# Performance work log

Measured on AMD Instinct MI355X. Metric: run time of the kernel, lower is better.

## Reference

```python
import jax, jax.numpy as jnp
import numpy as np

N_NODES = 50000
N_GRAPHS = 64
VOCAB = 100000
D = 256
PAD_IDX = 0


def setup_inputs() -> dict:
    key = jax.random.key(0)
    ks = jax.random.split(key, 8)
    seq = jax.random.randint(ks[0], (N_NODES, 16), 0, VOCAB)
    edge_index = jax.random.randint(ks[1], (2, 800000), 0, N_NODES)
    batch = jnp.sort(jax.random.randint(ks[2], (N_NODES,), 0, N_GRAPHS))
    emb = jax.random.normal(ks[3], (VOCAB, D), dtype=jnp.float32) * 0.02
    emb = emb.at[PAD_IDX].set(0.0)  # padding_idx row is zero
    W0 = jax.random.normal(ks[4], (D, D), dtype=jnp.float32) * (1.0 / np.sqrt(D))
    b0 = jnp.zeros((D,), dtype=jnp.float32)
    W1 = jax.random.normal(ks[5], (D, D), dtype=jnp.float32) * (1.0 / np.sqrt(D))
    b1 = jnp.zeros((D,), dtype=jnp.float32)
    return {"seq": seq, "edge_index": edge_index, "batch": batch,
            "emb": emb, "W0": W0, "b0": b0, "W1": W1, "b1": b1}


def _gcn_layer(x, W, b, src, dst, dis):
    # GCN with self-loops and symmetric normalization.
    h = x @ W + b  # [N, D]
    norm = dis[src] * dis[dst]  # [E]
    agg = jax.ops.segment_sum(h[src] * norm[:, None], dst, num_segments=N_NODES)
    agg = agg + h * (dis * dis)[:, None]  # self-loop contribution
    return agg


def reference(seq, edge_index, batch, emb, W0, b0, W1, b1):
    # statement encoder: embedding lookup + sum over token parts
    x = jnp.sum(emb[seq], axis=1)  # [N, D]
    src, dst = edge_index[0], edge_index[1]
    # degree with self-loops (counted on destination)
    deg = jax.ops.segment_sum(jnp.ones_like(dst, dtype=x.dtype), dst,
                              num_segments=N_NODES) + 1.0
    dis = jax.lax.rsqrt(deg)  # deg^{-1/2}
    h = _gcn_layer(x, W0, b0, src, dst, dis)
    h = jax.nn.relu(h)
    h = _gcn_layer(h, W1, b1, src, dst, dis)
    out = jax.nn.relu(h)
    # global sum pool over graph ids
    pooled = jax.ops.segment_sum(out, batch, num_segments=N_GRAPHS)  # [G, D]
    return pooled
```

## Files before the change

### kernel.cpp

```cpp
#include <hip/hip_runtime.h>
#include <stdint.h>

#define N_NODES 50000
#define N_GRAPHS 64
#define VOCAB 100000
#define DIM 256
#define N_EDGES 800000
#define T_SEQ 16
#define CAP 64

typedef short bf16x8 __attribute__((ext_vector_type(8)));
typedef unsigned short u16x8 __attribute__((ext_vector_type(8)));
typedef unsigned short u16x4 __attribute__((ext_vector_type(4)));
typedef float f32x4 __attribute__((ext_vector_type(4)));
typedef unsigned short u16;

__device__ __forceinline__ float bf2f(u16 u) {
    union { unsigned int i; float f; } v; v.i = ((unsigned int)u) << 16; return v.f;
}
__device__ __forceinline__ u16 f2bf(float f) {
    union { float f; unsigned int i; } v; v.f = f;
    unsigned int x = v.i;
    return (u16)((x + 0x7fffu + ((x >> 16) & 1u)) >> 16);
}

__device__ __forceinline__ void gload_lds16(const void* g, void* l) {
    __builtin_amdgcn_global_load_lds(
        (const __attribute__((address_space(1))) uint32_t*)g,
        (__attribute__((address_space(3))) uint32_t*)l, 16, 0, 0);
}

__global__ __launch_bounds__(256) void prep_kernel(const float* __restrict__ emb,
        u16* __restrict__ emb_bf, const float* __restrict__ W0, u16* __restrict__ WT0,
        const float* __restrict__ W1, u16* __restrict__ WT1,
        int* __restrict__ counts, float* __restrict__ out) {
    int bid = blockIdx.x;
    if (bid < 12500) {
        size_t base = ((size_t)bid * 256 + threadIdx.x) * 8;
        float4 a = *(const float4*)(emb + base);
        float4 b = *(const float4*)(emb + base + 4);
        ushort4 o0, o1;
        o0.x = f2bf(a.x); o0.y = f2bf(a.y); o0.z = f2bf(a.z); o0.w = f2bf(a.w);
        o1.x = f2bf(b.x); o1.y = f2bf(b.y); o1.z = f2bf(b.z); o1.w = f2bf(b.w);
        *(ushort4*)(emb_bf + base) = o0;
        *(ushort4*)(emb_bf + base + 4) = o1;
        if (bid < 196) {
            int i = bid * 256 + threadIdx.x;
            if (i < N_NODES) counts[i] = 0;
        }
        if (bid < 64) out[bid * 256 + threadIdx.x] = 0.f;
    } else {
        __shared__ u16 tile[32][33];
        int b = bid - 12500;
        int which = b >> 6;
        const float* W = which ? W1 : W0;
        u16* WT = which ? WT1 : WT0;
        b &= 63;
        int bx = b & 7, by = b >> 3;
        int tx = threadIdx.x & 31, ty = threadIdx.x >> 5;
#pragma unroll
        for (int r = 0; r < 32; r += 8)
            tile[ty + r][tx] = f2bf(W[(size_t)(by * 32 + ty + r) * DIM + bx * 32 + tx]);
        __syncthreads();
#pragma unroll
        for (int r = 0; r < 32; r += 8)
            WT[(size_t)(bx * 32 + ty + r) * DIM + by * 32 + tx] = tile[tx][ty + r];
    }
}

__global__ void fill_kernel(const int* __restrict__ src, const int* __restrict__ dst,
        int* __restrict__ counts, u16* __restrict__ bucket) {
    int e = blockIdx.x * 256 + threadIdx.x;
    if (e < N_EDGES) {
        int d = dst[e];
        int p = atomicAdd(&counts[d], 1);
        if (p < CAP) bucket[(size_t)d * CAP + p] = (u16)src[e];
    }
}

__global__ __launch_bounds__(256) void encode_kernel(const int* __restrict__ seq,
        const u16* __restrict__ emb, u16* __restrict__ x) {
    int wave = threadIdx.x >> 6, lane = threadIdx.x & 63;
    int n = blockIdx.x * 4 + wave;
    if (n >= N_NODES) return;
    int half = lane >> 5, l32 = lane & 31;
    int c = l32 * 8;
    int toks[8];
#pragma unroll
    for (int tt = 0; tt < 8; ++tt)
        toks[tt] = seq[n * T_SEQ + half + 2 * tt];
    u16x8 v[8];
#pragma unroll
    for (int tt = 0; tt < 8; ++tt)
        v[tt] = *(const u16x8*)(emb + (size_t)toks[tt] * DIM + c);
    __builtin_amdgcn_sched_barrier(0);
    float a[8] = {0.f, 0.f, 0.f, 0.f, 0.f, 0.f, 0.f, 0.f};
#pragma unroll
    for (int tt = 0; tt < 8; ++tt)
#pragma unroll
        for (int j = 0; j < 8; ++j) a[j] += bf2f(v[tt][j]);
#pragma unroll
    for (int j = 0; j < 8; ++j) a[j] += __shfl_xor(a[j], 32, 64);
    if (half == 0) {
        u16x8 o;
#pragma unroll
        for (int j = 0; j < 8; ++j) o[j] = f2bf(a[j]);
        *(u16x8*)(x + (size_t)n * DIM + c) = o;
    }
}

__global__ __launch_bounds__(256) void gemm_kernel(const u16* __restrict__ A,
        const u16* __restrict__ WT, const float* __restrict__ bias,
        const int* __restrict__ counts, u16* __restrict__ C, int M) {
    __shared__ __align__(16) uint8_t ldsA[128 * 64];
    __shared__ __align__(16) uint8_t ldsB[128 * 64];
    int tid = threadIdx.x;
    int wave = tid >> 6, lane = tid & 63;
    int quad = lane >> 4, l16 = lane & 15;
    int wm = wave & 1, wn = wave >> 1;
    int bm = blockIdx.y * 128, bn = blockIdx.x * 128;

    int srow = wave * 32 + (lane >> 2);
    int sbyte = (lane & 3) * 16;
    uint8_t* dstA = ldsA + wave * 2048;
    uint8_t* dstB = ldsB + wave * 2048;

    f32x4 acc[4][4] = {};

    for (int kt = 0; kt < 8; ++kt) {
        int k0b = kt * 64;
#pragma unroll
        for (int q = 0; q < 2; ++q) {
            int gr = bm + srow + q * 16; if (gr > M - 1) gr = M - 1;
            gload_lds16((const uint8_t*)A + (size_t)gr * (DIM * 2) + k0b + sbyte,
                        dstA + q * 1024);
            int gbr = bn + srow + q * 16;
            gload_lds16((const uint8_t*)WT + (size_t)gbr * (DIM * 2) + k0b + sbyte,
                        dstB + q * 1024);
        }
        __syncthreads();
        bf16x8 afr[4], bfr[4];
#pragma unroll
        for (int t = 0; t < 4; ++t) {
            afr[t] = *(const bf16x8*)(ldsA + (wm * 64 + t * 16 + l16) * 64 + quad * 16);
            bfr[t] = *(const bf16x8*)(ldsB + (wn * 64 + t * 16 + l16) * 64 + quad * 16);
        }
#pragma unroll
        for (int tm = 0; tm < 4; ++tm)
#pragma unroll
            for (int tn = 0; tn < 4; ++tn)
                acc[tm][tn] = __builtin_amdgcn_mfma_f32_16x16x32_bf16(
                    afr[tm], bfr[tn], acc[tm][tn], 0, 0, 0);
        __syncthreads();
    }

    float bv[4];
#pragma unroll
    for (int tn = 0; tn < 4; ++tn) bv[tn] = bias[bn + wn * 64 + tn * 16 + l16];
#pragma unroll
    for (int tm = 0; tm < 4; ++tm) {
        int row0 = bm + wm * 64 + tm * 16 + quad * 4;
#pragma unroll
        for (int r = 0; r < 4; ++r) {
            int row = row0 + r;
            if (row < M) {
                int cnt = counts[row]; if (cnt > CAP) cnt = CAP;
                float dsc = rsqrtf((float)cnt + 1.0f);
#pragma unroll
                for (int tn = 0; tn < 4; ++tn) {
                    int col = bn + wn * 64 + tn * 16 + l16;
                    C[(size_t)row * DIM + col] = f2bf((acc[tm][tn][r] + bv[tn]) * dsc);
                }
            }
        }
    }
}

__global__ __launch_bounds__(256) void agg_kernel(const u16* __restrict__ h,
        const int* __restrict__ counts, const u16* __restrict__ bucket,
        u16* __restrict__ z) {
    int wave = threadIdx.x >> 6, lane = threadIdx.x & 63;
    int n = blockIdx.x * 4 + wave;
    if (n >= N_NODES) return;
    int half = lane >> 5, l32 = lane & 31;
    int c = l32 * 8;
    float a[8];
    if (half == 0) {
        u16x8 v = *(const u16x8*)(h + (size_t)n * DIM + c);
#pragma unroll
        for (int j = 0; j < 8; ++j) a[j] = bf2f(v[j]);
    } else {
#pragma unroll
        for (int j = 0; j < 8; ++j) a[j] = 0.f;
    }
    int cnt = counts[n]; if (cnt > CAP) cnt = CAP;
    const u16* bk = bucket + (size_t)n * CAP;
    int e = half;
    for (; e + 14 < cnt; e += 16) {
        int s0 = bk[e];      int s1 = bk[e + 2];
        int s2 = bk[e + 4];  int s3 = bk[e + 6];
        int s4 = bk[e + 8];  int s5 = bk[e + 10];
        int s6 = bk[e + 12]; int s7 = bk[e + 14];
        u16x8 v0 = *(const u16x8*)(h + (size_t)s0 * DIM + c);
        u16x8 v1 = *(const u16x8*)(h + (size_t)s1 * DIM + c);
        u16x8 v2 = *(const u16x8*)(h + (size_t)s2 * DIM + c);
        u16x8 v3 = *(const u16x8*)(h + (size_t)s3 * DIM + c);
        u16x8 v4 = *(const u16x8*)(h + (size_t)s4 * DIM + c);
        u16x8 v5 = *(const u16x8*)(h + (size_t)s5 * DIM + c);
        u16x8 v6 = *(const u16x8*)(h + (size_t)s6 * DIM + c);
        u16x8 v7 = *(const u16x8*)(h + (size_t)s7 * DIM + c);
        __builtin_amdgcn_sched_barrier(0);
#pragma unroll
        for (int j = 0; j < 8; ++j)
            a[j] += ((bf2f(v0[j]) + bf2f(v1[j])) + (bf2f(v2[j]) + bf2f(v3[j]))) +
                    ((bf2f(v4[j]) + bf2f(v5[j])) + (bf2f(v6[j]) + bf2f(v7[j])));
    }
    for (; e + 6 < cnt; e += 8) {
        int s0 = bk[e];
        int s1 = bk[e + 2];
        int s2 = bk[e + 4];
        int s3 = bk[e + 6];
        u16x8 v0 = *(const u16x8*)(h + (size_t)s0 * DIM + c);
        u16x8 v1 = *(const u16x8*)(h + (size_t)s1 * DIM + c);
        u16x8 v2 = *(const u16x8*)(h + (size_t)s2 * DIM + c);
        u16x8 v3 = *(const u16x8*)(h + (size_t)s3 * DIM + c);
#pragma unroll
        for (int j = 0; j < 8; ++j)
            a[j] += bf2f(v0[j]) + bf2f(v1[j]) + bf2f(v2[j]) + bf2f(v3[j]);
    }
    for (; e < cnt; e += 2) {
        int s = bk[e];
        u16x8 v = *(const u16x8*)(h + (size_t)s * DIM + c);
#pragma unroll
        for (int j = 0; j < 8; ++j) a[j] += bf2f(v[j]);
    }
#pragma unroll
    for (int j = 0; j < 8; ++j) a[j] += __shfl_xor(a[j], 32, 64);
    if (half == 0) {
        float dn = rsqrtf((float)cnt + 1.0f);
        u16x8 o;
#pragma unroll
        for (int j = 0; j < 8; ++j) o[j] = f2bf(fmaxf(a[j] * dn, 0.f));
        *(u16x8*)(z + (size_t)n * DIM + c) = o;
    }
}

__global__ __launch_bounds__(256) void pool_kernel(const u16* __restrict__ z,
        const int* __restrict__ batch, float* __restrict__ out) {
    const int NWAVES = 4096;
    const int NPW = (N_NODES + NWAVES - 1) / NWAVES;
    int gw = blockIdx.x * 4 + (threadIdx.x >> 6);
    int lane = threadIdx.x & 63;
    int n0 = gw * NPW;
    if (n0 >= N_NODES) return;
    int n1 = n0 + NPW; if (n1 > N_NODES) n1 = N_NODES;
    int c = lane * 4;
    float a0 = 0.f, a1 = 0.f, a2 = 0.f, a3 = 0.f;
    int gprev = -1;
    for (int n = n0; n < n1; ++n) {
        int g = batch[n];
        if (g != gprev) {
            if (gprev >= 0) {
                float* o = out + (size_t)gprev * DIM + c;
                atomicAdd(o + 0, a0); atomicAdd(o + 1, a1);
                atomicAdd(o + 2, a2); atomicAdd(o + 3, a3);
            }
            a0 = a1 = a2 = a3 = 0.f; gprev = g;
        }
        u16x4 v = *(const u16x4*)(z + (size_t)n * DIM + c);
        a0 += bf2f(v[0]); a1 += bf2f(v[1]); a2 += bf2f(v[2]); a3 += bf2f(v[3]);
    }
    if (gprev >= 0) {
        float* o = out + (size_t)gprev * DIM + c;
        atomicAdd(o + 0, a0); atomicAdd(o + 1, a1);
        atomicAdd(o + 2, a2); atomicAdd(o + 3, a3);
    }
}

extern "C" void kernel_launch(void* const* d_in, const int* in_sizes, int n_in,
                              void* d_out, int out_size, void* d_ws, size_t ws_size,
                              hipStream_t stream) {
    const int*   seq   = (const int*)d_in[0];
    const int*   eidx  = (const int*)d_in[1];
    const int*   batch = (const int*)d_in[2];
    const float* emb   = (const float*)d_in[3];
    const float* W0    = (const float*)d_in[4];
    const float* b0    = (const float*)d_in[5];
    const float* W1    = (const float*)d_in[6];
    const float* b1    = (const float*)d_in[7];
    float* out = (float*)d_out;

    uint8_t* ws = (uint8_t*)d_ws;
    size_t off = 0;
    auto alloc = [&](size_t bytes) -> uint8_t* {
        uint8_t* p = ws + off;
        off += (bytes + 255) & ~(size_t)255;
        return p;
    };
    u16* emb_bf  = (u16*)alloc((size_t)VOCAB * DIM * 2);
    u16* buf0    = (u16*)alloc((size_t)N_NODES * DIM * 2);
    u16* buf1    = (u16*)alloc((size_t)N_NODES * DIM * 2);
    u16* bucket  = (u16*)alloc((size_t)N_NODES * CAP * 2);
    int* counts  = (int*)alloc((size_t)N_NODES * 4);
    u16* WT0     = (u16*)alloc((size_t)DIM * DIM * 2);
    u16* WT1     = (u16*)alloc((size_t)DIM * DIM * 2);

    const int* esrc = eidx;
    const int* edst = eidx + N_EDGES;

    prep_kernel<<<12500 + 128, 256, 0, stream>>>(emb, emb_bf, W0, WT0, W1, WT1,
                                                 counts, out);
    fill_kernel<<<(N_EDGES + 255) / 256, 256, 0, stream>>>(esrc, edst, counts, bucket);
    encode_kernel<<<(N_NODES + 3) / 4, 256, 0, stream>>>(seq, emb_bf, buf0);

    dim3 ggrid(2, (N_NODES + 127) / 128);
    gemm_kernel<<<ggrid, 256, 0, stream>>>(buf0, WT0, b0, counts, buf1, N_NODES);
    agg_kernel<<<(N_NODES + 3) / 4, 256, 0, stream>>>(buf1, counts, bucket, buf0);
    gemm_kernel<<<ggrid, 256, 0, stream>>>(buf0, WT1, b1, counts, buf1, N_NODES);
    agg_kernel<<<(N_NODES + 3) / 4, 256, 0, stream>>>(buf1, counts, bucket, buf0);

    pool_kernel<<<1024, 256, 0, stream>>>(buf0, batch, out);
}
```

Before: 442.0 us.

## Fuse edge bucketing into prep kernel and fuse final aggregation with pooling

Edge bucket filling now runs as extra blocks inside the prep/cast kernel, and the counts and output zeroing moves to memset calls. The second aggregation is fused with global sum pooling, so each wave aggregates a run of nodes and accumulates per graph in registers instead of writing z and re-reading it. This saves one launch pair and a full N×D round trip. The cost is fewer waves in the fused agg/pool (2048 blocks, several nodes per wave serially), which may reduce latency hiding for the gathers.

```diff
diff --git a/kernel.cpp b/kernel.cpp
--- a/kernel.cpp
+++ b/kernel.cpp
@@ -9,6 +9,13 @@
 #define T_SEQ 16
 #define CAP 64
 
+#define FILL_BLOCKS 3125
+#define CAST_BLOCKS 12500
+#define TRAN_BLOCKS 128
+
+#define AP_BLOCKS 2048
+#define AP_NPW ((N_NODES + AP_BLOCKS * 4 - 1) / (AP_BLOCKS * 4))
+
 typedef short bf16x8 __attribute__((ext_vector_type(8)));
 typedef unsigned short u16x8 __attribute__((ext_vector_type(8)));
 typedef unsigned short u16x4 __attribute__((ext_vector_type(4)));
@@ -30,13 +37,19 @@
         (__attribute__((address_space(3))) uint32_t*)l, 16, 0, 0);
 }
 
-__global__ __launch_bounds__(256) void prep_kernel(const float* __restrict__ emb,
+__global__ __launch_bounds__(256) void prep_fill_kernel(const float* __restrict__ emb,
         u16* __restrict__ emb_bf, const float* __restrict__ W0, u16* __restrict__ WT0,
         const float* __restrict__ W1, u16* __restrict__ WT1,
-        int* __restrict__ counts, float* __restrict__ out) {
+        const int* __restrict__ esrc, const int* __restrict__ edst,
+        int* __restrict__ counts, u16* __restrict__ bucket) {
     int bid = blockIdx.x;
-    if (bid < 12500) {
-        size_t base = ((size_t)bid * 256 + threadIdx.x) * 8;
+    if (bid < FILL_BLOCKS) {
+        int e = bid * 256 + threadIdx.x;
+        int d = edst[e];
+        int p = atomicAdd(&counts[d], 1);
+        if (p < CAP) bucket[(size_t)d * CAP + p] = (u16)esrc[e];
+    } else if (bid < FILL_BLOCKS + CAST_BLOCKS) {
+        size_t base = ((size_t)(bid - FILL_BLOCKS) * 256 + threadIdx.x) * 8;
         float4 a = *(const float4*)(emb + base);
         float4 b = *(const float4*)(emb + base + 4);
         ushort4 o0, o1;
@@ -44,14 +57,9 @@
         o1.x = f2bf(b.x); o1.y = f2bf(b.y); o1.z = f2bf(b.z); o1.w = f2bf(b.w);
         *(ushort4*)(emb_bf + base) = o0;
         *(ushort4*)(emb_bf + base + 4) = o1;
-        if (bid < 196) {
-            int i = bid * 256 + threadIdx.x;
-            if (i < N_NODES) counts[i] = 0;
-        }
-        if (bid < 64) out[bid * 256 + threadIdx.x] = 0.f;
     } else {
         __shared__ u16 tile[32][33];
-        int b = bid - 12500;
+        int b = bid - (FILL_BLOCKS + CAST_BLOCKS);
         int which = b >> 6;
         const float* W = which ? W1 : W0;
         u16* WT = which ? WT1 : WT0;
@@ -65,16 +73,6 @@
 #pragma unroll
         for (int r = 0; r < 32; r += 8)
             WT[(size_t)(bx * 32 + ty + r) * DIM + by * 32 + tx] = tile[tx][ty + r];
-    }
-}
-
-__global__ void fill_kernel(const int* __restrict__ src, const int* __restrict__ dst,
-        int* __restrict__ counts, u16* __restrict__ bucket) {
-    int e = blockIdx.x * 256 + threadIdx.x;
-    if (e < N_EDGES) {
-        int d = dst[e];
-        int p = atomicAdd(&counts[d], 1);
-        if (p < CAP) bucket[(size_t)d * CAP + p] = (u16)src[e];
     }
 }
 
@@ -176,15 +174,9 @@
     }
 }
 
-__global__ __launch_bounds__(256) void agg_kernel(const u16* __restrict__ h,
-        const int* __restrict__ counts, const u16* __restrict__ bucket,
-        u16* __restrict__ z) {
-    int wave = threadIdx.x >> 6, lane = threadIdx.x & 63;
-    int n = blockIdx.x * 4 + wave;
-    if (n >= N_NODES) return;
-    int half = lane >> 5, l32 = lane & 31;
-    int c = l32 * 8;
-    float a[8];
+__device__ __forceinline__ void agg_node(int n, int half, int c,
+        const u16* __restrict__ h, const int* __restrict__ counts,
+        const u16* __restrict__ bucket, float a[8]) {
     if (half == 0) {
         u16x8 v = *(const u16x8*)(h + (size_t)n * DIM + c);
 #pragma unroll
@@ -216,10 +208,8 @@
                     ((bf2f(v4[j]) + bf2f(v5[j])) + (bf2f(v6[j]) + bf2f(v7[j])));
     }
     for (; e + 6 < cnt; e += 8) {
-        int s0 = bk[e];
-        int s1 = bk[e + 2];
-        int s2 = bk[e + 4];
-        int s3 = bk[e + 6];
+        int s0 = bk[e];     int s1 = bk[e + 2];
+        int s2 = bk[e + 4]; int s3 = bk[e + 6];
         u16x8 v0 = *(const u16x8*)(h + (size_t)s0 * DIM + c);
         u16x8 v1 = *(const u16x8*)(h + (size_t)s1 * DIM + c);
         u16x8 v2 = *(const u16x8*)(h + (size_t)s2 * DIM + c);
@@ -236,44 +226,62 @@
     }
 #pragma unroll
     for (int j = 0; j < 8; ++j) a[j] += __shfl_xor(a[j], 32, 64);
+    float dn = rsqrtf((float)cnt + 1.0f);
+#pragma unroll
+    for (int j = 0; j < 8; ++j) a[j] = fmaxf(a[j] * dn, 0.f);
+}
+
+__global__ __launch_bounds__(256) void agg_kernel(const u16* __restrict__ h,
+        const int* __restrict__ counts, const u16* __restrict__ bucket,
+        u16* __restrict__ z) {
+    int wave = threadIdx.x >> 6, lane = threadIdx.x & 63;
+    int n = blockIdx.x * 4 + wave;
+    if (n >= N_NODES) return;
+    int half = lane >> 5, l32 = lane & 31;
+    int c = l32 * 8;
+    float a[8];
+    agg_node(n, half, c, h, counts, bucket, a);
     if (half == 0) {
-        float dn = rsqrtf((float)cnt + 1.0f);
         u16x8 o;
 #pragma unroll
-        for (int j = 0; j < 8; ++j) o[j] = f2bf(fmaxf(a[j] * dn, 0.f));
+        for (int j = 0; j < 8; ++j) o[j] = f2bf(a[j]);
         *(u16x8*)(z + (size_t)n * DIM + c) = o;
     }
 }
 
-__global__ __launch_bounds__(256) void pool_kernel(const u16* __restrict__ z,
+__global__ __launch_bounds__(256) void agg_pool_kernel(const u16* __restrict__ h,
+        const int* __restrict__ counts, const u16* __restrict__ bucket,
         const int* __restrict__ batch, float* __restrict__ out) {
-    const int NWAVES = 4096;
-    const int NPW = (N_NODES + NWAVES - 1) / NWAVES;
     int gw = blockIdx.x * 4 + (threadIdx.x >> 6);
     int lane = threadIdx.x & 63;
-    int n0 = gw * NPW;
+    int half = lane >> 5, l32 = lane & 31;
+    int c = l32 * 8;
+    int n0 = gw * AP_NPW;
     if (n0 >= N_NODES) return;
-    int n1 = n0 + NPW; if (n1 > N_NODES) n1 = N_NODES;
-    int c = lane * 4;
-    float a0 = 0.f, a1 = 0.f, a2 = 0.f, a3 = 0.f;
+    int n1 = n0 + AP_NPW; if (n1 > N_NODES) n1 = N_NODES;
+    float pacc[8] = {0.f, 0.f, 0.f, 0.f, 0.f, 0.f, 0.f, 0.f};
     int gprev = -1;
     for (int n = n0; n < n1; ++n) {
+        float a[8];
+        agg_node(n, half, c, h, counts, bucket, a);
         int g = batch[n];
         if (g != gprev) {
-            if (gprev >= 0) {
+            if (gprev >= 0 && half == 0) {
                 float* o = out + (size_t)gprev * DIM + c;
-                atomicAdd(o + 0, a0); atomicAdd(o + 1, a1);
-                atomicAdd(o + 2, a2); atomicAdd(o + 3, a3);
+#pragma unroll
+                for (int j = 0; j < 8; ++j) atomicAdd(o + j, pacc[j]);
             }
-            a0 = a1 = a2 = a3 = 0.f; gprev = g;
+#pragma unroll
+            for (int j = 0; j < 8; ++j) pacc[j] = 0.f;
+            gprev = g;
         }
-        u16x4 v = *(const u16x4*)(z + (size_t)n * DIM + c);
-        a0 += bf2f(v[0]); a1 += bf2f(v[1]); a2 += bf2f(v[2]); a3 += bf2f(v[3]);
-    }
-    if (gprev >= 0) {
+#pragma unroll
+        for (int j = 0; j < 8; ++j) pacc[j] += a[j];
+    }
+    if (gprev >= 0 && half == 0) {
         float* o = out + (size_t)gprev * DIM + c;
-        atomicAdd(o + 0, a0); atomicAdd(o + 1, a1);
-        atomicAdd(o + 2, a2); atomicAdd(o + 3, a3);
+#pragma unroll
+        for (int j = 0; j < 8; ++j) atomicAdd(o + j, pacc[j]);
     }
 }
 
@@ -308,16 +316,16 @@
     const int* esrc = eidx;
     const int* edst = eidx + N_EDGES;
 
-    prep_kernel<<<12500 + 128, 256, 0, stream>>>(emb, emb_bf, W0, WT0, W1, WT1,
-                                                 counts, out);
-    fill_kernel<<<(N_EDGES + 255) / 256, 256, 0, stream>>>(esrc, edst, counts, bucket);
+    hipMemsetAsync(counts, 0, (size_t)N_NODES * 4, stream);
+    hipMemsetAsync(out, 0, (size_t)N_GRAPHS * DIM * 4, stream);
+
+    prep_fill_kernel<<<FILL_BLOCKS + CAST_BLOCKS + TRAN_BLOCKS, 256, 0, stream>>>(
+        emb, emb_bf, W0, WT0, W1, WT1, esrc, edst, counts, bucket);
     encode_kernel<<<(N_NODES + 3) / 4, 256, 0, stream>>>(seq, emb_bf, buf0);
 
     dim3 ggrid(2, (N_NODES + 127) / 128);
     gemm_kernel<<<ggrid, 256, 0, stream>>>(buf0, WT0, b0, counts, buf1, N_NODES);
     agg_kernel<<<(N_NODES + 3) / 4, 256, 0, stream>>>(buf1, counts, bucket, buf0);
     gemm_kernel<<<ggrid, 256, 0, stream>>>(buf0, WT1, b1, counts, buf1, N_NODES);
-    agg_kernel<<<(N_NODES + 3) / 4, 256, 0, stream>>>(buf1, counts, bucket, buf0);
-
-    pool_kernel<<<1024, 256, 0, stream>>>(buf0, batch, out);
-}
+    agg_pool_kernel<<<AP_BLOCKS, 256, 0, stream>>>(buf1, counts, bucket, batch, out);
+}
```

After: 485.5 us. 9.8% more time.

## Fuse edge bucketing into prep kernel and double-buffer GEMM LDS tiles

Applied to the files above, without the earlier changes.

Merges the edge-bucket fill kernel into the embedding-cast/weight-transpose prep kernel so both run as independent block ranges of one launch. Zeroing of counts and the output moves to hipMemsetAsync calls. The GEMM now double-buffers its LDS A/B tiles, issuing the next k-tile's global-to-LDS loads before computing on the current one, with source addresses hoisted out of the loop. This trades two extra memset launches and twice the LDS per block for fewer kernel launches and overlap of loads with MFMA work. The shown loop no longer has a barrier between issuing the next loads and the MFMAs, so correctness depends on the hidden tail of the loop adding a wait and sync.

```diff
diff --git a/kernel.cpp b/kernel.cpp
--- a/kernel.cpp
+++ b/kernel.cpp
@@ -9,6 +9,10 @@
 #define T_SEQ 16
 #define CAP 64
 
+#define FILL_BLOCKS 3125
+#define CAST_BLOCKS 12500
+#define TRAN_BLOCKS 128
+
 typedef short bf16x8 __attribute__((ext_vector_type(8)));
 typedef unsigned short u16x8 __attribute__((ext_vector_type(8)));
 typedef unsigned short u16x4 __attribute__((ext_vector_type(4)));
@@ -30,13 +34,19 @@
         (__attribute__((address_space(3))) uint32_t*)l, 16, 0, 0);
 }
 
-__global__ __launch_bounds__(256) void prep_kernel(const float* __restrict__ emb,
+__global__ __launch_bounds__(256) void prep_fill_kernel(const float* __restrict__ emb,
         u16* __restrict__ emb_bf, const float* __restrict__ W0, u16* __restrict__ WT0,
         const float* __restrict__ W1, u16* __restrict__ WT1,
-        int* __restrict__ counts, float* __restrict__ out) {
+        const int* __restrict__ esrc, const int* __restrict__ edst,
+        int* __restrict__ counts, u16* __restrict__ bucket) {
     int bid = blockIdx.x;
-    if (bid < 12500) {
-        size_t base = ((size_t)bid * 256 + threadIdx.x) * 8;
+    if (bid < FILL_BLOCKS) {
+        int e = bid * 256 + threadIdx.x;
+        int d = edst[e];
+        int p = atomicAdd(&counts[d], 1);
+        if (p < CAP) bucket[(size_t)d * CAP + p] = (u16)esrc[e];
+    } else if (bid < FILL_BLOCKS + CAST_BLOCKS) {
+        size_t base = ((size_t)(bid - FILL_BLOCKS) * 256 + threadIdx.x) * 8;
         float4 a = *(const float4*)(emb + base);
         float4 b = *(const float4*)(emb + base + 4);
         ushort4 o0, o1;
@@ -44,14 +54,9 @@
         o1.x = f2bf(b.x); o1.y = f2bf(b.y); o1.z = f2bf(b.z); o1.w = f2bf(b.w);
         *(ushort4*)(emb_bf + base) = o0;
         *(ushort4*)(emb_bf + base + 4) = o1;
-        if (bid < 196) {
-            int i = bid * 256 + threadIdx.x;
-            if (i < N_NODES) counts[i] = 0;
-        }
-        if (bid < 64) out[bid * 256 + threadIdx.x] = 0.f;
     } else {
         __shared__ u16 tile[32][33];
-        int b = bid - 12500;
+        int b = bid - (FILL_BLOCKS + CAST_BLOCKS);
         int which = b >> 6;
         const float* W = which ? W1 : W0;
         u16* WT = which ? WT1 : WT0;
@@ -65,16 +70,6 @@
 #pragma unroll
         for (int r = 0; r < 32; r += 8)
             WT[(size_t)(bx * 32 + ty + r) * DIM + by * 32 + tx] = tile[tx][ty + r];
-    }
-}
-
-__global__ void fill_kernel(const int* __restrict__ src, const int* __restrict__ dst,
-        int* __restrict__ counts, u16* __restrict__ bucket) {
-    int e = blockIdx.x * 256 + threadIdx.x;
-    if (e < N_EDGES) {
-        int d = dst[e];
-        int p = atomicAdd(&counts[d], 1);
-        if (p < CAP) bucket[(size_t)d * CAP + p] = (u16)src[e];
     }
 }
 
@@ -112,8 +107,8 @@
 __global__ __launch_bounds__(256) void gemm_kernel(const u16* __restrict__ A,
         const u16* __restrict__ WT, const float* __restrict__ bias,
         const int* __restrict__ counts, u16* __restrict__ C, int M) {
-    __shared__ __align__(16) uint8_t ldsA[128 * 64];
-    __shared__ __align__(16) uint8_t ldsB[128 * 64];
+    __shared__ __align__(16) uint8_t ldsA[2][128 * 64];
+    __shared__ __align__(16) uint8_t ldsB[2][128 * 64];
     int tid = threadIdx.x;
     int wave = tid >> 6, lane = tid & 63;
     int quad = lane >> 4, l16 = lane & 15;
@@ -122,28 +117,36 @@
 
     int srow = wave * 32 + (lane >> 2);
     int sbyte = (lane & 3) * 16;
-    uint8_t* dstA = ldsA + wave * 2048;
-    uint8_t* dstB = ldsB + wave * 2048;
+    int grA0 = bm + srow;      if (grA0 > M - 1) grA0 = M - 1;
+    int grA1 = bm + srow + 16; if (grA1 > M - 1) grA1 = M - 1;
+    const uint8_t* Asrc0 = (const uint8_t*)A + (size_t)grA0 * (DIM * 2) + sbyte;
+    const uint8_t* Asrc1 = (const uint8_t*)A + (size_t)grA1 * (DIM * 2) + sbyte;
+    const uint8_t* Bsrc0 = (const uint8_t*)WT + (size_t)(bn + srow) * (DIM * 2) + sbyte;
+    const uint8_t* Bsrc1 = (const uint8_t*)WT + (size_t)(bn + srow + 16) * (DIM * 2) + sbyte;
+    int woff = wave * 2048;
 
     f32x4 acc[4][4] = {};
 
+    gload_lds16(Asrc0, ldsA[0] + woff);
+    gload_lds16(Asrc1, ldsA[0] + woff + 1024);
+    gload_lds16(Bsrc0, ldsB[0] + woff);
+    gload_lds16(Bsrc1, ldsB[0] + woff + 1024);
+    __syncthreads();
+
     for (int kt = 0; kt < 8; ++kt) {
-        int k0b = kt * 64;
-#pragma unroll
-        for (int q = 0; q < 2; ++q) {
-            int gr = bm + srow + q * 16; if (gr > M - 1) gr = M - 1;
-            gload_lds16((const uint8_t*)A + (size_t)gr * (DIM * 2) + k0b + sbyte,
-                        dstA + q * 1024);
-            int gbr = bn + srow + q * 16;
-            gload_lds16((const uint8_t*)WT + (size_t)gbr * (DIM * 2) + k0b + sbyte,
-                        dstB + q * 1024);
+        int cur = kt & 1, nxt = cur ^ 1;
+        if (kt < 7) {
+            int k1b = (kt + 1) * 64;
+            gload_lds16(Asrc0 + k1b, ldsA[nxt] + woff);
+            gload_lds16(Asrc1 + k1b, ldsA[nxt] + woff + 1024);
+            gload_lds16(Bsrc0 + k1b, ldsB[nxt] + woff);
+            gload_lds16(Bsrc1 + k1b, ldsB[nxt] + woff + 1024);
         }
-        __syncthreads();
         bf16x8 afr[4], bfr[4];
 #pragma unroll
         for (int t = 0; t < 4; ++t) {
-            afr[t] = *(const bf16x8*)(ldsA + (wm * 64 + t * 16 + l16) * 64 + quad * 16);
-            bfr[t] = *(const bf16x8*)(ldsB + (wn * 64 + t * 16 + l16) * 64 + quad * 16);
+            afr[t] = *(const bf16x8*)(ldsA[cur] + (wm * 64 + t * 16 + l16) * 64 + quad * 16);
+            bfr[t] = *(const bf16x8*)(ldsB[cur] + (wn * 64 + t * 16 + l16) * 64 + quad * 16);
         }
 #pragma unroll
         for (int tm = 0; tm < 4; ++tm)
@@ -216,10 +219,8 @@
                     ((bf2f(v4[j]) + bf2f(v5[j])) + (bf2f(v6[j]) + bf2f(v7[j])));
     }
     for (; e + 6 < cnt; e += 8) {
-        int s0 = bk[e];
-        int s1 = bk[e + 2];
-        int s2 = bk[e + 4];
-        int s3 = bk[e + 6];
+        int s0 = bk[e];     int s1 = bk[e + 2];
+        int s2 = bk[e + 4]; int s3 = bk[e + 6];
         u16x8 v0 = *(const u16x8*)(h + (size_t)s0 * DIM + c);
         u16x8 v1 = *(const u16x8*)(h + (size_t)s1 * DIM + c);
         u16x8 v2 = *(const u16x8*)(h + (size_t)s2 * DIM + c);
@@ -308,9 +309,11 @@
     const int* esrc = eidx;
     const int* edst = eidx + N_EDGES;
 
-    prep_kernel<<<12500 + 128, 256, 0, stream>>>(emb, emb_bf, W0, WT0, W1, WT1,
-                                                 counts, out);
-    fill_kernel<<<(N_EDGES + 255) / 256, 256, 0, stream>>>(esrc, edst, counts, bucket);
+    hipMemsetAsync(counts, 0, (size_t)N_NODES * 4, stream);
+    hipMemsetAsync(out, 0, (size_t)N_GRAPHS * DIM * 4, stream);
+
+    prep_fill_kernel<<<FILL_BLOCKS + CAST_BLOCKS + TRAN_BLOCKS, 256, 0, stream>>>(
+        emb, emb_bf, W0, WT0, W1, WT1, esrc, edst, counts, bucket);
     encode_kernel<<<(N_NODES + 3) / 4, 256, 0, stream>>>(seq, emb_bf, buf0);
 
     dim3 ggrid(2, (N_NODES + 127) / 128);
```

New measurement: 446.4 us. About the same (+1.0%).
